# Kernel tuning notes

Measured on AMD Instinct MI355X. Metric: run time of the kernel, lower is better.

Reference implementation:

```python
import jax, jax.numpy as jnp
import numpy as np

D_MODEL = 768
N_HEADS = 8
HEAD_DIM = D_MODEL // N_HEADS
LN_EPS = 1e-5

def setup_inputs() -> dict:
    key = jax.random.key(0)
    k1, k2, k3 = jax.random.split(key, 3)
    B, L = 8, 4096
    x = jax.random.normal(k1, (B, L, D_MODEL), dtype=jnp.float32)
    gamma = jnp.ones((D_MODEL,), dtype=jnp.float32)
    beta = jnp.zeros((D_MODEL,), dtype=jnp.float32)
    # torch Linear weights transposed so forward is x @ W
    w_qkv = jax.random.normal(k2, (D_MODEL, 3 * D_MODEL), dtype=jnp.float32) * (1.0 / np.sqrt(D_MODEL))
    w_out = jax.random.normal(k3, (D_MODEL, D_MODEL), dtype=jnp.float32) * (1.0 / np.sqrt(D_MODEL))
    return {"x": x, "gamma": gamma, "beta": beta, "w_qkv": w_qkv, "w_out": w_out}

def reference(x, gamma, beta, w_qkv, w_out):
    B, L, D = x.shape
    residual = x
    # LayerNorm
    mu = jnp.mean(x, axis=-1, keepdims=True)
    var = jnp.mean(jnp.square(x - mu), axis=-1, keepdims=True)
    xn = (x - mu) * jax.lax.rsqrt(var + LN_EPS) * gamma + beta
    # qkv projection, split, reshape to [B, H, L, d]
    qkv = xn @ w_qkv  # [B, L, 3D]
    q, k, v = jnp.split(qkv, 3, axis=-1)
    def to_heads(t):
        return t.reshape(B, L, N_HEADS, HEAD_DIM).transpose(0, 2, 1, 3)
    q, k, v = to_heads(q), to_heads(k), to_heads(v)
    # feature maps: elu + 1
    q = jax.nn.elu(q) + 1.0
    k = jax.nn.elu(k) + 1.0
    # linear attention: kv aggregation then query readout
    kv = jnp.einsum('bhld,bhlv->bhdv', k, v)          # [B,H,d,d]
    out = jnp.einsum('bhld,bhdv->bhlv', q, kv)         # [B,H,L,d]
    k_sum = jnp.sum(k, axis=2)                         # [B,H,d]
    normalizer = jnp.einsum('bhld,bhd->bhl', q, k_sum) # [B,H,L]
    normalizer = jnp.maximum(normalizer, 1e-6)
    out = out / normalizer[..., None]
    out = out.transpose(0, 2, 1, 3).reshape(B, L, D)
    out = out @ w_out
    return out + residual
```

## Files before the change

### kernel.cpp

```cpp
#include <hip/hip_runtime.h>
#include <stdint.h>

#define D_MODEL 768
#define N3      2304
#define NHEAD   8
#define DH      96
#define BATCH   8
#define SEQ     4096
#define ROWS    (BATCH*SEQ)
#define LN_EPS  1e-5f

typedef __attribute__((ext_vector_type(8))) __bf16 bf16x8;
typedef __attribute__((ext_vector_type(4))) float f32x4;
typedef __attribute__((ext_vector_type(8))) unsigned short ushort8;
typedef __attribute__((ext_vector_type(4))) unsigned short ushort4v;

__device__ __forceinline__ unsigned short f2bf(float f) {
  union { float f; unsigned int u; } v; v.f = f;
  unsigned int r = v.u + 0x7FFFu + ((v.u >> 16) & 1u);
  return (unsigned short)(r >> 16);
}
__device__ __forceinline__ float bf2f(unsigned short u) {
  union { unsigned int u; float f; } v; v.u = ((unsigned int)u) << 16;
  return v.f;
}

#define GLOBAL_LDS16(src, dst) \
  __builtin_amdgcn_global_load_lds((const __attribute__((address_space(1))) void*)(src), \
                                   (__attribute__((address_space(3))) void*)(dst), 16, 0, 0)

#define GATE(n) do { asm volatile("s_waitcnt vmcnt(" #n ")" ::: "memory"); \
                     __builtin_amdgcn_s_barrier(); asm volatile("" ::: "memory"); } while (0)

__global__ __launch_bounds__(256) void transpose_cast_kernel(
    const float* __restrict__ in, unsigned short* __restrict__ out, int R, int C) {
  __shared__ float tile[32][33];
  int c0 = blockIdx.x * 32, r0 = blockIdx.y * 32;
  int tx = threadIdx.x & 31, ty = threadIdx.x >> 5;
  #pragma unroll
  for (int i = ty; i < 32; i += 8)
    tile[i][tx] = in[(size_t)(r0 + i) * C + c0 + tx];
  __syncthreads();
  #pragma unroll
  for (int i = ty; i < 32; i += 8)
    out[(size_t)(c0 + i) * R + r0 + tx] = f2bf(tile[tx][i]);
}

__global__ __launch_bounds__(256) void ln_kernel(
    const float* __restrict__ x, const float* __restrict__ gamma,
    const float* __restrict__ beta, unsigned short* __restrict__ xn) {
  int wave = threadIdx.x >> 6, lane = threadIdx.x & 63;
  int row = blockIdx.x * 4 + wave;
  const float* xr = x + (size_t)row * D_MODEL;
  f32x4 v[3];
  float s = 0.f, sq = 0.f;
  #pragma unroll
  for (int i = 0; i < 3; ++i) {
    v[i] = *(const f32x4*)(xr + (i * 64 + lane) * 4);
    #pragma unroll
    for (int c = 0; c < 4; ++c) { s += v[i][c]; sq += v[i][c] * v[i][c]; }
  }
  #pragma unroll
  for (int o = 32; o; o >>= 1) {
    s  += __shfl_xor(s, o, 64);
    sq += __shfl_xor(sq, o, 64);
  }
  float mu  = s * (1.f / 768.f);
  float var = sq * (1.f / 768.f) - mu * mu;
  float rs  = rsqrtf(var + LN_EPS);
  #pragma unroll
  for (int i = 0; i < 3; ++i) {
    int col = (i * 64 + lane) * 4;
    ushort4v o;
    #pragma unroll
    for (int c = 0; c < 4; ++c)
      o[c] = f2bf((v[i][c] - mu) * rs * gamma[col + c] + beta[col + c]);
    *(ushort4v*)(xn + (size_t)row * D_MODEL + col) = o;
  }
}

__global__ __launch_bounds__(512, 2) void gemm_qkv_kernel(
    const unsigned short* __restrict__ A, const unsigned short* __restrict__ Bt,
    unsigned short* __restrict__ qb, unsigned short* __restrict__ kT,
    unsigned short* __restrict__ vT) {
  __shared__ unsigned short As[3 * 8192];
  __shared__ unsigned short Bs[3 * 8192];
  const int K = D_MODEL, NKT = 24, nbn = N3 / 256;
  int nwg = gridDim.x, id = blockIdx.x;
  int q8 = nwg >> 3;
  int wg = (id & 7) * q8 + (id >> 3);
  int bm = wg / nbn, bn = wg % nbn;

  const int lane = threadIdx.x & 63, wid = threadIdx.x >> 6;
  const int wm = wid >> 2, wn = wid & 3;
  const int l15 = lane & 15, hi = lane >> 4;
  const int colS = (hi ^ ((l15 >> 1) & 3)) << 3;
  const int srow = lane >> 2;
  const int scol = ((lane & 3) ^ ((lane >> 3) & 3)) << 3;

  auto stage = [&](unsigned short* dstBase, const unsigned short* G, int bOff,
                   int buf, int kt) {
    #pragma unroll
    for (int q = 0; q < 2; ++q) {
      const unsigned short* src =
          G + (size_t)(bOff * 256 + q * 128 + wid * 16 + srow) * K + kt * 32 + scol;
      GLOBAL_LDS16(src, dstBase + buf * 8192 + q * 4096 + wid * 512);
    }
  };

  f32x4 acc[8][4];
  #pragma unroll
  for (int i = 0; i < 8; ++i)
    #pragma unroll
    for (int j = 0; j < 4; ++j) acc[i][j] = (f32x4){0.f, 0.f, 0.f, 0.f};

#define QTILE(BUF, STG) do { \
    bf16x8 af[8], bv[4]; \
    _Pragma("unroll") for (int mf = 0; mf < 8; ++mf) \
      af[mf] = *(const bf16x8*)&As[(BUF) * 8192 + (wm * 128 + mf * 16 + l15) * 32 + colS]; \
    _Pragma("unroll") for (int nf = 0; nf < 4; ++nf) \
      bv[nf] = *(const bf16x8*)&Bs[(BUF) * 8192 + (wn * 64 + nf * 16 + l15) * 32 + colS]; \
    STG; \
    __builtin_amdgcn_s_setprio(1); \
    _Pragma("unroll") for (int mf = 0; mf < 8; ++mf) \
      _Pragma("unroll") for (int nf = 0; nf < 4; ++nf) \
        acc[mf][nf] = __builtin_amdgcn_mfma_f32_16x16x32_bf16( \
            af[mf], bv[nf], acc[mf][nf], 0, 0, 0); \
    __builtin_amdgcn_s_setprio(0); \
  } while (0)

  stage(As, A, bm, 0, 0); stage(Bs, Bt, bn, 0, 0);
  stage(As, A, bm, 1, 1); stage(Bs, Bt, bn, 1, 1);

  for (int it = 0; it < 7; ++it) {
    int T = 3 * it;
    GATE(4); QTILE(0, { stage(As, A, bm, 2, T + 2); stage(Bs, Bt, bn, 2, T + 2); });
    GATE(4); QTILE(1, { stage(As, A, bm, 0, T + 3); stage(Bs, Bt, bn, 0, T + 3); });
    GATE(4); QTILE(2, { stage(As, A, bm, 1, T + 4); stage(Bs, Bt, bn, 1, T + 4); });
  }
  GATE(4); QTILE(0, { stage(As, A, bm, 2, NKT - 1); stage(Bs, Bt, bn, 2, NKT - 1); });
  GATE(4); QTILE(1, {});
  GATE(0); QTILE(2, {});
#undef QTILE

  int r0 = bm * 256 + wm * 128, c0 = bn * 256 + wn * 64;
  #pragma unroll
  for (int mf = 0; mf < 8; ++mf) {
    int lr = r0 + mf * 16 + hi * 4;
    int b = lr >> 12, lloc = lr & 4095;
    #pragma unroll
    for (int nf = 0; nf < 4; ++nf) {
      int col = c0 + nf * 16 + l15;
      float vv[4];
      #pragma unroll
      for (int r = 0; r < 4; ++r) {
        float v = acc[mf][nf][r];
        if (col < 1536) v = (v > 0.f) ? v + 1.f : __expf(v);
        vv[r] = v;
      }
      if (col < 768) {
        #pragma unroll
        for (int r = 0; r < 4; ++r)
          qb[(size_t)(lr + r) * D_MODEL + col] = f2bf(vv[r]);
      } else {
        int cc = (col < 1536) ? col - 768 : col - 1536;
        int h = cc / 96, d = cc - h * 96;
        unsigned short* T = (col < 1536) ? kT : vT;
        ushort4v pk = {f2bf(vv[0]), f2bf(vv[1]), f2bf(vv[2]), f2bf(vv[3])};
        *(ushort4v*)&T[((size_t)(b * 8 + h) * 96 + d) * 4096 + lloc] = pk;
      }
    }
  }
}

__global__ __launch_bounds__(256, 3) void gemm_out_kernel(
    const unsigned short* __restrict__ A, const unsigned short* __restrict__ Bt,
    const float* __restrict__ resid, float* __restrict__ Cf) {
  __shared__ unsigned short As[3 * 4096];
  __shared__ unsigned short Bs[3 * 4096];
  const int K = D_MODEL, nbn = 6;
  int nwg = gridDim.x, id = blockIdx.x;
  int q8 = nwg >> 3;
  int wg = (id & 7) * q8 + (id >> 3);
  int bm = wg / nbn, bn = wg % nbn;

  const int lane = threadIdx.x & 63, wid = threadIdx.x >> 6;
  const int wm = wid >> 1, wn = wid & 1;
  const int l15 = lane & 15, hi = lane >> 4;
  const int colS = (hi ^ ((l15 >> 1) & 3)) << 3;
  const int srow = lane >> 2;
  const int scol = ((lane & 3) ^ ((lane >> 3) & 3)) << 3;

  const unsigned short* a0 = A  + (size_t)(bm * 128 +      wid * 16 + srow) * K + scol;
  const unsigned short* a1 = A  + (size_t)(bm * 128 + 64 + wid * 16 + srow) * K + scol;
  const unsigned short* b0 = Bt + (size_t)(bn * 128 +      wid * 16 + srow) * K + scol;
  const unsigned short* b1 = Bt + (size_t)(bn * 128 + 64 + wid * 16 + srow) * K + scol;
  auto stage = [&](int buf, int kt) {
    GLOBAL_LDS16(a0 + kt * 32, &As[buf * 4096 +        wid * 512]);
    GLOBAL_LDS16(a1 + kt * 32, &As[buf * 4096 + 2048 + wid * 512]);
    GLOBAL_LDS16(b0 + kt * 32, &Bs[buf * 4096 +        wid * 512]);
    GLOBAL_LDS16(b1 + kt * 32, &Bs[buf * 4096 + 2048 + wid * 512]);
  };

  f32x4 acc[4][4];
  #pragma unroll
  for (int i = 0; i < 4; ++i)
    #pragma unroll
    for (int j = 0; j < 4; ++j) acc[i][j] = (f32x4){0.f, 0.f, 0.f, 0.f};

#define HTILE(BUF, STG) do { \
    bf16x8 af[4], bv[4]; \
    _Pragma("unroll") for (int mf = 0; mf < 4; ++mf) \
      af[mf] = *(const bf16x8*)&As[(BUF) * 4096 + (wm * 64 + mf * 16 + l15) * 32 + colS]; \
    _Pragma("unroll") for (int nf = 0; nf < 4; ++nf) \
      bv[nf] = *(const bf16x8*)&Bs[(BUF) * 4096 + (wn * 64 + nf * 16 + l15) * 32 + colS]; \
    STG; \
    __builtin_amdgcn_s_setprio(1); \
    _Pragma("unroll") for (int mf = 0; mf < 4; ++mf) \
      _Pragma("unroll") for (int nf = 0; nf < 4; ++nf) \
        acc[mf][nf] = __builtin_amdgcn_mfma_f32_16x16x32_bf16( \
            af[mf], bv[nf], acc[mf][nf], 0, 0, 0); \
    __builtin_amdgcn_s_setprio(0); \
  } while (0)

  stage(0, 0); stage(1, 1);
  for (int it = 0; it < 7; ++it) {
    int T = 3 * it;
    GATE(4); HTILE(0, stage(2, T + 2));
    GATE(4); HTILE(1, stage(0, T + 3));
    GATE(4); HTILE(2, stage(1, T + 4));
  }
  GATE(4); HTILE(0, stage(2, 23));
  GATE(4); HTILE(1, {});
  GATE(0); HTILE(2, {});
#undef HTILE

  int r0 = bm * 128 + wm * 64, c0 = bn * 128 + wn * 64;
  #pragma unroll
  for (int mf = 0; mf < 4; ++mf)
    #pragma unroll
    for (int nf = 0; nf < 4; ++nf) {
      int col = c0 + nf * 16 + l15;
      #pragma unroll
      for (int r = 0; r < 4; ++r) {
        int row = r0 + mf * 16 + hi * 4 + r;
        Cf[(size_t)row * D_MODEL + col] =
            acc[mf][nf][r] + resid[(size_t)row * D_MODEL + col];
      }
    }
}

__global__ __launch_bounds__(256) void kvagg2_kernel(
    const unsigned short* __restrict__ kT, const unsigned short* __restrict__ vT,
    float* __restrict__ kvp) {
  __shared__ unsigned short KTs[3 * 6144];
  __shared__ unsigned short VTs[3 * 8192];
  int bh = blockIdx.x >> 2, chunk = blockIdx.x & 3;
  int tid = threadIdx.x;
  int lane = tid & 63, wid = tid >> 6;
  int l15 = lane & 15, hi = lane >> 4;

  #pragma unroll
  for (int i = 0; i < 3; ++i) {
    int s = i * 256 + tid;
    int buf = s >> 8, r = 96 + ((s >> 3) & 31), sl = s & 7;
    unsigned short val = (r == 96) ? (unsigned short)0x3F80 : (unsigned short)0;
    ushort8 v8 = {val, val, val, val, val, val, val, val};
    *(ushort8*)&VTs[buf * 8192 + r * 64 + sl * 8] = v8;
  }
  __syncthreads();

  const size_t kbase = ((size_t)bh * 96) * 4096 + chunk * 1024;
  auto stage = [&](int buf, int t) {
    #pragma unroll
    for (int i = 0; i < 3; ++i) {
      int sidx = i * 256 + tid;
      int row = sidx >> 3;
      int L = (sidx & 7) ^ (row & 7);
      size_t g = kbase + (size_t)row * 4096 + t * 64 + L * 8;
      GLOBAL_LDS16(kT + g, &KTs[buf * 6144 + (i * 256 + wid * 64) * 8]);
      GLOBAL_LDS16(vT + g, &VTs[buf * 8192 + (i * 256 + wid * 64) * 8]);
    }
  };

  f32x4 acc[6][2];
  #pragma unroll
  for (int i = 0; i < 6; ++i)
    #pragma unroll
    for (int j = 0; j < 2; ++j) acc[i][j] = (f32x4){0.f, 0.f, 0.f, 0.f};

#define KVTILE(BUF) do { \
    _Pragma("unroll") for (int kq = 0; kq < 2; ++kq) { \
      bf16x8 af[6], bv[2]; \
      _Pragma("unroll") for (int mf = 0; mf < 6; ++mf) { \
        int row = mf * 16 + l15; \
        af[mf] = *(const bf16x8*)&KTs[(BUF) * 6144 + row * 64 + ((kq * 4 + hi) ^ (row & 7)) * 8]; } \
      _Pragma("unroll") for (int nf = 0; nf < 2; ++nf) { \
        int row = wid * 32 + nf * 16 + l15; \
        bv[nf] = *(const bf16x8*)&VTs[(BUF) * 8192 + row * 64 + ((kq * 4 + hi) ^ (row & 7)) * 8]; } \
      __builtin_amdgcn_s_setprio(1); \
      _Pragma("unroll") for (int mf = 0; mf < 6; ++mf) \
        _Pragma("unroll") for (int nf = 0; nf < 2; ++nf) \
          acc[mf][nf] = __builtin_amdgcn_mfma_f32_16x16x32_bf16( \
              af[mf], bv[nf], acc[mf][nf], 0, 0, 0); \
      __builtin_amdgcn_s_setprio(0); \
    } } while (0)

  stage(0, 0); stage(1, 1);
  for (int t = 0; t < 14; ++t) {
    stage((t + 2) % 3, t + 2);
    GATE(12);
    KVTILE(t % 3);
  }
  GATE(6); KVTILE(2);
  GATE(0); KVTILE(0);
#undef KVTILE

  float* outp = kvp + ((size_t)bh * 4 + chunk) * (96 * 112);
  #pragma unroll
  for (int nf = 0; nf < 2; ++nf) {
    int e = wid * 32 + nf * 16 + l15;
    if (e < 112) {
      #pragma unroll
      for (int mf = 0; mf < 6; ++mf)
        #pragma unroll
        for (int r = 0; r < 4; ++r) {
          int d = mf * 16 + hi * 4 + r;
          outp[d * 112 + e] = acc[mf][nf][r];
        }
    }
  }
}

__global__ __launch_bounds__(256) void kvreduce_kernel(
    const float* __restrict__ kvp, unsigned short* __restrict__ kvTo) {
  int idx = blockIdx.x * 256 + threadIdx.x;
  if (idx >= 64 * 112 * 96) return;
  int d = idx % 96;
  int e = (idx / 96) % 112;
  int bh = idx / (96 * 112);
  float s = 0.f;
  #pragma unroll
  for (int c = 0; c < 4; ++c)
    s += kvp[(((size_t)bh * 4 + c) * 96 + d) * 112 + e];
  kvTo[idx] = f2bf(s);
}

__global__ __launch_bounds__(256) void readout_kernel(
    const unsigned short* __restrict__ qb, const unsigned short* __restrict__ kvT,
    unsigned short* __restrict__ attn) {
  __shared__ unsigned short Qs[128][104];
  __shared__ unsigned short Ks[112][104];
  int bh = blockIdx.x >> 5, lc = blockIdx.x & 31;
  int b = bh >> 3, h = bh & 7;
  int l0 = lc * 128;
  int wave = threadIdx.x >> 6, lane = threadIdx.x & 63;
  #pragma unroll
  for (int i = 0; i < 6; ++i) {
    int idx = i * 256 + threadIdx.x;
    int l = idx / 12, oc = idx % 12;
    size_t g = ((size_t)b * SEQ + l0 + l) * D_MODEL + h * DH + oc * 8;
    *(ushort8*)&Qs[l][oc * 8] = *(const ushort8*)(qb + g);
  }
  const unsigned short* kvbh = kvT + (size_t)bh * 112 * 96;
  #pragma unroll
  for (int i = 0; i < 6; ++i) {
    int idx = i * 256 + threadIdx.x;
    if (idx < 1344) {
      int e = idx / 12, oc = idx % 12;
      *(ushort8*)&Ks[e][oc * 8] = *(const ushort8*)(kvbh + e * 96 + oc * 8);
    }
  }
  __syncthreads();
  f32x4 acc[2][7];
  #pragma unroll
  for (int i = 0; i < 2; ++i)
    #pragma unroll
    for (int j = 0; j < 7; ++j) acc[i][j] = (f32x4){0.f, 0.f, 0.f, 0.f};
  #pragma unroll
  for (int kq = 0; kq < 3; ++kq) {
    int k0 = kq * 32 + (lane >> 4) * 8;
    bf16x8 af[2], bfv[7];
    #pragma unroll
    for (int i = 0; i < 2; ++i) af[i]  = *(const bf16x8*)&Qs[wave * 32 + i * 16 + (lane & 15)][k0];
    #pragma unroll
    for (int j = 0; j < 7; ++j) bfv[j] = *(const bf16x8*)&Ks[j * 16 + (lane & 15)][k0];
    #pragma unroll
    for (int i = 0; i < 2; ++i)
      #pragma unroll
      for (int j = 0; j < 7; ++j)
        acc[i][j] = __builtin_amdgcn_mfma_f32_16x16x32_bf16(af[i], bfv[j], acc[i][j], 0, 0, 0);
  }
  int g4 = lane >> 4;
  #pragma unroll
  for (int i = 0; i < 2; ++i) {
    #pragma unroll
    for (int r = 0; r < 4; ++r) {
      float nv = __shfl(acc[i][6][r], lane & 48, 64);
      float inv = 1.f / fmaxf(nv, 1e-6f);
      size_t orow = (size_t)b * SEQ + l0 + wave * 32 + i * 16 + g4 * 4 + r;
      #pragma unroll
      for (int j = 0; j < 6; ++j) {
        int col = h * DH + j * 16 + (lane & 15);
        attn[orow * D_MODEL + col] = f2bf(acc[i][j][r] * inv);
      }
    }
  }
}

extern "C" void kernel_launch(void* const* d_in, const int* in_sizes, int n_in,
                              void* d_out, int out_size, void* d_ws, size_t ws_size,
                              hipStream_t stream) {
  const float* x     = (const float*)d_in[0];
  const float* gamma = (const float*)d_in[1];
  const float* beta  = (const float*)d_in[2];
  const float* w_qkv = (const float*)d_in[3];
  const float* w_out = (const float*)d_in[4];
  float* out = (float*)d_out;

  char* ws = (char*)d_ws;
  size_t off = 0;
  auto alloc = [&](size_t bytes) -> void* {
    void* p = ws + off; off += (bytes + 255) & ~(size_t)255; return p;
  };
  unsigned short* xn    = (unsigned short*)alloc((size_t)ROWS * D_MODEL * 2);
  unsigned short* qb    = (unsigned short*)alloc((size_t)ROWS * D_MODEL * 2);
  unsigned short* kTb   = (unsigned short*)alloc((size_t)64 * 96 * SEQ * 2);
  unsigned short* vTb   = (unsigned short*)alloc((size_t)64 * 96 * SEQ * 2);
  unsigned short* wqkvT = (unsigned short*)alloc((size_t)N3 * D_MODEL * 2);
  unsigned short* woutT = (unsigned short*)alloc((size_t)D_MODEL * D_MODEL * 2);
  float* kvp            = (float*)alloc((size_t)256 * 96 * 112 * 4);
  unsigned short* kvT   = (unsigned short*)alloc((size_t)64 * 112 * 96 * 2);

  transpose_cast_kernel<<<dim3(N3 / 32, D_MODEL / 32), 256, 0, stream>>>(w_qkv, wqkvT, D_MODEL, N3);
  transpose_cast_kernel<<<dim3(D_MODEL / 32, D_MODEL / 32), 256, 0, stream>>>(w_out, woutT, D_MODEL, D_MODEL);
  ln_kernel<<<ROWS / 4, 256, 0, stream>>>(x, gamma, beta, xn);
  gemm_qkv_kernel<<<(ROWS / 256) * (N3 / 256), 512, 0, stream>>>(xn, wqkvT, qb, kTb, vTb);
  kvagg2_kernel<<<256, 256, 0, stream>>>(kTb, vTb, kvp);
  kvreduce_kernel<<<(64 * 112 * 96 + 255) / 256, 256, 0, stream>>>(kvp, kvT);
  readout_kernel<<<2048, 256, 0, stream>>>(qb, kvT, xn);
  gemm_out_kernel<<<(ROWS / 128) * (D_MODEL / 128), 256, 0, stream>>>(xn, woutT, x, out);
}
```

Measured before the change: 340.2 us.

## Restructure QKV GEMM into 8-phase ping-pong schedule with BK=64 double buffering

```diff
diff --git a/kernel.cpp b/kernel.cpp
--- a/kernel.cpp
+++ b/kernel.cpp
@@ -29,8 +29,11 @@
   __builtin_amdgcn_global_load_lds((const __attribute__((address_space(1))) void*)(src), \
                                    (__attribute__((address_space(3))) void*)(dst), 16, 0, 0)
 
+#define BAR2() do { asm volatile("" ::: "memory"); __builtin_amdgcn_s_barrier(); \
+                    asm volatile("" ::: "memory"); } while (0)
 #define GATE(n) do { asm volatile("s_waitcnt vmcnt(" #n ")" ::: "memory"); \
                      __builtin_amdgcn_s_barrier(); asm volatile("" ::: "memory"); } while (0)
+#define LGKM0() asm volatile("s_waitcnt lgkmcnt(0)" ::: "memory")
 
 __global__ __launch_bounds__(256) void transpose_cast_kernel(
     const float* __restrict__ in, unsigned short* __restrict__ out, int R, int C) {
@@ -79,13 +82,14 @@
   }
 }
 
-__global__ __launch_bounds__(512, 2) void gemm_qkv_kernel(
+__global__ __launch_bounds__(512, 2) void gemm_qkv8_kernel(
     const unsigned short* __restrict__ A, const unsigned short* __restrict__ Bt,
     unsigned short* __restrict__ qb, unsigned short* __restrict__ kT,
     unsigned short* __restrict__ vT) {
-  __shared__ unsigned short As[3 * 8192];
-  __shared__ unsigned short Bs[3 * 8192];
-  const int K = D_MODEL, NKT = 24, nbn = N3 / 256;
+  __shared__ unsigned short As[2 * 16384];
+  __shared__ unsigned short Bs[2 * 16384];
+  const int K = D_MODEL, NKT = 12, nbn = N3 / 256;
+
   int nwg = gridDim.x, id = blockIdx.x;
   int q8 = nwg >> 3;
   int wg = (id & 7) * q8 + (id >> 3);
@@ -94,83 +98,121 @@
   const int lane = threadIdx.x & 63, wid = threadIdx.x >> 6;
   const int wm = wid >> 2, wn = wid & 3;
   const int l15 = lane & 15, hi = lane >> 4;
-  const int colS = (hi ^ ((l15 >> 1) & 3)) << 3;
-  const int srow = lane >> 2;
-  const int scol = ((lane & 3) ^ ((lane >> 3) & 3)) << 3;
-
-  auto stage = [&](unsigned short* dstBase, const unsigned short* G, int bOff,
-                   int buf, int kt) {
+  const int rsw = (hi ^ (l15 & 7)) << 3;
+  const int scol = ((lane & 7) ^ (lane >> 3)) << 3;
+
+  auto stgA = [&](int buf, int h, int kt) {
     #pragma unroll
     for (int q = 0; q < 2; ++q) {
+      int rbase = h * 128 + q * 64 + wid * 8;
       const unsigned short* src =
-          G + (size_t)(bOff * 256 + q * 128 + wid * 16 + srow) * K + kt * 32 + scol;
-      GLOBAL_LDS16(src, dstBase + buf * 8192 + q * 4096 + wid * 512);
+          A + (size_t)(bm * 256 + rbase + (lane >> 3)) * K + kt * 64 + scol;
+      GLOBAL_LDS16(src, &As[buf * 16384 + rbase * 64]);
     }
   };
-
-  f32x4 acc[8][4];
-  #pragma unroll
-  for (int i = 0; i < 8; ++i)
-    #pragma unroll
-    for (int j = 0; j < 4; ++j) acc[i][j] = (f32x4){0.f, 0.f, 0.f, 0.f};
-
-#define QTILE(BUF, STG) do { \
-    bf16x8 af[8], bv[4]; \
-    _Pragma("unroll") for (int mf = 0; mf < 8; ++mf) \
-      af[mf] = *(const bf16x8*)&As[(BUF) * 8192 + (wm * 128 + mf * 16 + l15) * 32 + colS]; \
-    _Pragma("unroll") for (int nf = 0; nf < 4; ++nf) \
-      bv[nf] = *(const bf16x8*)&Bs[(BUF) * 8192 + (wn * 64 + nf * 16 + l15) * 32 + colS]; \
-    STG; \
-    __builtin_amdgcn_s_setprio(1); \
-    _Pragma("unroll") for (int mf = 0; mf < 8; ++mf) \
-      _Pragma("unroll") for (int nf = 0; nf < 4; ++nf) \
-        acc[mf][nf] = __builtin_amdgcn_mfma_f32_16x16x32_bf16( \
-            af[mf], bv[nf], acc[mf][nf], 0, 0, 0); \
-    __builtin_amdgcn_s_setprio(0); \
-  } while (0)
-
-  stage(As, A, bm, 0, 0); stage(Bs, Bt, bn, 0, 0);
-  stage(As, A, bm, 1, 1); stage(Bs, Bt, bn, 1, 1);
-
-  for (int it = 0; it < 7; ++it) {
-    int T = 3 * it;
-    GATE(4); QTILE(0, { stage(As, A, bm, 2, T + 2); stage(Bs, Bt, bn, 2, T + 2); });
-    GATE(4); QTILE(1, { stage(As, A, bm, 0, T + 3); stage(Bs, Bt, bn, 0, T + 3); });
-    GATE(4); QTILE(2, { stage(As, A, bm, 1, T + 4); stage(Bs, Bt, bn, 1, T + 4); });
-  }
-  GATE(4); QTILE(0, { stage(As, A, bm, 2, NKT - 1); stage(Bs, Bt, bn, 2, NKT - 1); });
-  GATE(4); QTILE(1, {});
-  GATE(0); QTILE(2, {});
-#undef QTILE
-
-  int r0 = bm * 256 + wm * 128, c0 = bn * 256 + wn * 64;
-  #pragma unroll
-  for (int mf = 0; mf < 8; ++mf) {
-    int lr = r0 + mf * 16 + hi * 4;
-    int b = lr >> 12, lloc = lr & 4095;
-    #pragma unroll
-    for (int nf = 0; nf < 4; ++nf) {
-      int col = c0 + nf * 16 + l15;
-      float vv[4];
-      #pragma unroll
-      for (int r = 0; r < 4; ++r) {
-        float v = acc[mf][nf][r];
-        if (col < 1536) v = (v > 0.f) ? v + 1.f : __expf(v);
-        vv[r] = v;
-      }
-      if (col < 768) {
+  auto stgB = [&](int buf, int h, int kt) {
+    #pragma unroll
+    for (int q = 0; q < 2; ++q) {
+      int rbase = h * 128 + q * 64 + wid * 8;
+      const unsigned short* src =
+          Bt + (size_t)(bn * 256 + rbase + (lane >> 3)) * K + kt * 64 + scol;
+      GLOBAL_LDS16(src, &Bs[buf * 16384 + rbase * 64]);
+    }
+  };
+
+  f32x4 acc[2][4][2][2];
+  #pragma unroll
+  for (int a = 0; a < 2; ++a)
+    #pragma unroll
+    for (int b = 0; b < 4; ++b)
+      #pragma unroll
+      for (int c = 0; c < 2; ++c)
         #pragma unroll
-        for (int r = 0; r < 4; ++r)
-          qb[(size_t)(lr + r) * D_MODEL + col] = f2bf(vv[r]);
-      } else {
-        int cc = (col < 1536) ? col - 768 : col - 1536;
-        int h = cc / 96, d = cc - h * 96;
-        unsigned short* T = (col < 1536) ? kT : vT;
-        ushort4v pk = {f2bf(vv[0]), f2bf(vv[1]), f2bf(vv[2]), f2bf(vv[3])};
-        *(ushort4v*)&T[((size_t)(b * 8 + h) * 96 + d) * 4096 + lloc] = pk;
-      }
-    }
-  }
+        for (int d = 0; d < 2; ++d) acc[a][b][c][d] = (f32x4){0.f, 0.f, 0.f, 0.f};
+
+  bf16x8 af[4][2], bv0[2][2], bv1[2][2];
+
+#define RDA(BUF, QM) do { _Pragma("unroll") \
+  for (int mf = 0; mf < 4; ++mf) { \
+    int r = wm * 128 + (QM) * 64 + mf * 16 + l15; \
+    int base = (BUF) * 16384 + r * 64 + rsw; \
+    af[mf][0] = *(const bf16x8*)&As[base]; \
+    af[mf][1] = *(const bf16x8*)&As[base ^ 32]; } } while (0)
+#define RDB(BUF, QN, BV) do { _Pragma("unroll") \
+  for (int nf = 0; nf < 2; ++nf) { \
+    int r = wn * 64 + (QN) * 32 + nf * 16 + l15; \
+    int base = (BUF) * 16384 + r * 64 + rsw; \
+    BV[nf][0] = *(const bf16x8*)&Bs[base]; \
+    BV[nf][1] = *(const bf16x8*)&Bs[base ^ 32]; } } while (0)
+#define MM(QM, QN, BV) do { __builtin_amdgcn_s_setprio(1); \
+  _Pragma("unroll") for (int mf = 0; mf < 4; ++mf) \
+  _Pragma("unroll") for (int nf = 0; nf < 2; ++nf) { \
+    acc[QM][mf][QN][nf] = __builtin_amdgcn_mfma_f32_16x16x32_bf16( \
+        af[mf][0], BV[nf][0], acc[QM][mf][QN][nf], 0, 0, 0); \
+    acc[QM][mf][QN][nf] = __builtin_amdgcn_mfma_f32_16x16x32_bf16( \
+        af[mf][1], BV[nf][1], acc[QM][mf][QN][nf], 0, 0, 0); } \
+  __builtin_amdgcn_s_setprio(0); } while (0)
+
+  stgA(0, 0, 0); stgA(0, 1, 0); stgB(0, 0, 0); stgB(0, 1, 0);
+  stgB(1, 0, 1); stgB(1, 1, 1);
+  GATE(4);
+
+  const int NITER = NKT >> 1;
+  for (int it = 0; it < NITER - 1; ++it) {
+    int T = 2 * it;
+    RDA(0, 0); RDB(0, 0, bv0); stgA(1, 0, T + 1); BAR2(); LGKM0(); MM(0, 0, bv0); BAR2();
+    RDB(0, 1, bv1);            stgA(1, 1, T + 1); BAR2(); LGKM0(); MM(0, 1, bv1); BAR2();
+    RDA(0, 1);                 stgB(0, 0, T + 2); BAR2(); LGKM0(); MM(1, 1, bv1); BAR2();
+                               stgB(0, 1, T + 2); BAR2();          MM(1, 0, bv0); GATE(4);
+    RDA(1, 0); RDB(1, 0, bv0); stgA(0, 0, T + 2); BAR2(); LGKM0(); MM(0, 0, bv0); BAR2();
+    RDB(1, 1, bv1);            stgA(0, 1, T + 2); BAR2(); LGKM0(); MM(0, 1, bv1); BAR2();
+    RDA(1, 1);                 stgB(1, 0, T + 3); BAR2(); LGKM0(); MM(1, 1, bv1); BAR2();
+                               stgB(1, 1, T + 3); BAR2();          MM(1, 0, bv0); GATE(4);
+  }
+  RDA(0, 0); RDB(0, 0, bv0); stgA(1, 0, NKT - 1); BAR2(); LGKM0(); MM(0, 0, bv0); BAR2();
+  RDB(0, 1, bv1);            stgA(1, 1, NKT - 1); BAR2(); LGKM0(); MM(0, 1, bv1); BAR2();
+  RDA(0, 1);                                      BAR2(); LGKM0(); MM(1, 1, bv1); BAR2();
+                                                  BAR2();          MM(1, 0, bv0); GATE(0);
+  RDA(1, 0); RDB(1, 0, bv0);                      BAR2(); LGKM0(); MM(0, 0, bv0); BAR2();
+  RDB(1, 1, bv1);                                 BAR2(); LGKM0(); MM(0, 1, bv1); BAR2();
+  RDA(1, 1);                                      BAR2(); LGKM0(); MM(1, 1, bv1); BAR2();
+                                                  BAR2();          MM(1, 0, bv0);
+#undef RDA
+#undef RDB
+#undef MM
+
+  int r0 = bm * 256 + wm * 128, c0b = bn * 256 + wn * 64;
+  #pragma unroll
+  for (int qm = 0; qm < 2; ++qm)
+    #pragma unroll
+    for (int mf = 0; mf < 4; ++mf) {
+      int lr = r0 + qm * 64 + mf * 16 + hi * 4;
+      int b = lr >> 12, lloc = lr & 4095;
+      #pragma unroll
+      for (int qn = 0; qn < 2; ++qn)
+        #pragma unroll
+        for (int nf = 0; nf < 2; ++nf) {
+          int col = c0b + qn * 32 + nf * 16 + l15;
+          float vv[4];
+          #pragma unroll
+          for (int r = 0; r < 4; ++r) {
+            float v = acc[qm][mf][qn][nf][r];
+            if (col < 1536) v = (v > 0.f) ? v + 1.f : __expf(v);
+            vv[r] = v;
+          }
+          if (col < 768) {
+            #pragma unroll
+            for (int r = 0; r < 4; ++r)
+              qb[(size_t)(lr + r) * D_MODEL + col] = f2bf(vv[r]);
+          } else {
+            int cc = (col < 1536) ? col - 768 : col - 1536;
+            int h = cc / 96, d = cc - h * 96;
+            unsigned short* T = (col < 1536) ? kT : vT;
+            ushort4v pk = {f2bf(vv[0]), f2bf(vv[1]), f2bf(vv[2]), f2bf(vv[3])};
+            *(ushort4v*)&T[((size_t)(b * 8 + h) * 96 + d) * 4096 + lloc] = pk;
+          }
+        }
+    }
 }
 
 __global__ __launch_bounds__(256, 3) void gemm_out_kernel(
@@ -435,7 +477,7 @@
   transpose_cast_kernel<<<dim3(N3 / 32, D_MODEL / 32), 256, 0, stream>>>(w_qkv, wqkvT, D_MODEL, N3);
   transpose_cast_kernel<<<dim3(D_MODEL / 32, D_MODEL / 32), 256, 0, stream>>>(w_out, woutT, D_MODEL, D_MODEL);
   ln_kernel<<<ROWS / 4, 256, 0, stream>>>(x, gamma, beta, xn);
-  gemm_qkv_kernel<<<(ROWS / 256) * (N3 / 256), 512, 0, stream>>>(xn, wqkvT, qb, kTb, vTb);
+  gemm_qkv8_kernel<<<(ROWS / 256) * (N3 / 256), 512, 0, stream>>>(xn, wqkvT, qb, kTb, vTb);
   kvagg2_kernel<<<256, 256, 0, stream>>>(kTb, vTb, kvp);
   kvreduce_kernel<<<(64 * 112 * 96 + 255) / 256, 256, 0, stream>>>(kvp, kvT);
   readout_kernel<<<2048, 256, 0, stream>>>(qb, kvT, xn);
```

After: 342.6 us. Within noise of the previous version (+0.7%).

## Shrink QKV GEMM tile to 128x128 with 4 waves and specialized epilogues

Applied to the files above, without the earlier changes.

```diff
diff --git a/kernel.cpp b/kernel.cpp
--- a/kernel.cpp
+++ b/kernel.cpp
@@ -79,94 +79,103 @@
   }
 }
 
-__global__ __launch_bounds__(512, 2) void gemm_qkv_kernel(
+__global__ __launch_bounds__(256, 3) void gemm_qkv128_kernel(
     const unsigned short* __restrict__ A, const unsigned short* __restrict__ Bt,
     unsigned short* __restrict__ qb, unsigned short* __restrict__ kT,
     unsigned short* __restrict__ vT) {
-  __shared__ unsigned short As[3 * 8192];
-  __shared__ unsigned short Bs[3 * 8192];
-  const int K = D_MODEL, NKT = 24, nbn = N3 / 256;
+  __shared__ unsigned short As[3 * 4096];
+  __shared__ unsigned short Bs[3 * 4096];
+  const int K = D_MODEL, nbn = 18;
   int nwg = gridDim.x, id = blockIdx.x;
   int q8 = nwg >> 3;
   int wg = (id & 7) * q8 + (id >> 3);
   int bm = wg / nbn, bn = wg % nbn;
 
   const int lane = threadIdx.x & 63, wid = threadIdx.x >> 6;
-  const int wm = wid >> 2, wn = wid & 3;
+  const int wm = wid >> 1, wn = wid & 1;
   const int l15 = lane & 15, hi = lane >> 4;
   const int colS = (hi ^ ((l15 >> 1) & 3)) << 3;
   const int srow = lane >> 2;
   const int scol = ((lane & 3) ^ ((lane >> 3) & 3)) << 3;
 
-  auto stage = [&](unsigned short* dstBase, const unsigned short* G, int bOff,
-                   int buf, int kt) {
-    #pragma unroll
-    for (int q = 0; q < 2; ++q) {
-      const unsigned short* src =
-          G + (size_t)(bOff * 256 + q * 128 + wid * 16 + srow) * K + kt * 32 + scol;
-      GLOBAL_LDS16(src, dstBase + buf * 8192 + q * 4096 + wid * 512);
-    }
+  const unsigned short* a0 = A  + (size_t)(bm * 128 +      wid * 16 + srow) * K + scol;
+  const unsigned short* a1 = A  + (size_t)(bm * 128 + 64 + wid * 16 + srow) * K + scol;
+  const unsigned short* b0 = Bt + (size_t)(bn * 128 +      wid * 16 + srow) * K + scol;
+  const unsigned short* b1 = Bt + (size_t)(bn * 128 + 64 + wid * 16 + srow) * K + scol;
+  auto stage = [&](int buf, int kt) {
+    GLOBAL_LDS16(a0 + kt * 32, &As[buf * 4096 +        wid * 512]);
+    GLOBAL_LDS16(a1 + kt * 32, &As[buf * 4096 + 2048 + wid * 512]);
+    GLOBAL_LDS16(b0 + kt * 32, &Bs[buf * 4096 +        wid * 512]);
+    GLOBAL_LDS16(b1 + kt * 32, &Bs[buf * 4096 + 2048 + wid * 512]);
   };
 
-  f32x4 acc[8][4];
-  #pragma unroll
-  for (int i = 0; i < 8; ++i)
+  f32x4 acc[4][4];
+  #pragma unroll
+  for (int i = 0; i < 4; ++i)
     #pragma unroll
     for (int j = 0; j < 4; ++j) acc[i][j] = (f32x4){0.f, 0.f, 0.f, 0.f};
 
 #define QTILE(BUF, STG) do { \
-    bf16x8 af[8], bv[4]; \
-    _Pragma("unroll") for (int mf = 0; mf < 8; ++mf) \
-      af[mf] = *(const bf16x8*)&As[(BUF) * 8192 + (wm * 128 + mf * 16 + l15) * 32 + colS]; \
+    bf16x8 af[4], bv[4]; \
+    _Pragma("unroll") for (int mf = 0; mf < 4; ++mf) \
+      af[mf] = *(const bf16x8*)&As[(BUF) * 4096 + (wm * 64 + mf * 16 + l15) * 32 + colS]; \
     _Pragma("unroll") for (int nf = 0; nf < 4; ++nf) \
-      bv[nf] = *(const bf16x8*)&Bs[(BUF) * 8192 + (wn * 64 + nf * 16 + l15) * 32 + colS]; \
+      bv[nf] = *(const bf16x8*)&Bs[(BUF) * 4096 + (wn * 64 + nf * 16 + l15) * 32 + colS]; \
     STG; \
     __builtin_amdgcn_s_setprio(1); \
-    _Pragma("unroll") for (int mf = 0; mf < 8; ++mf) \
+    _Pragma("unroll") for (int mf = 0; mf < 4; ++mf) \
       _Pragma("unroll") for (int nf = 0; nf < 4; ++nf) \
         acc[mf][nf] = __builtin_amdgcn_mfma_f32_16x16x32_bf16( \
             af[mf], bv[nf], acc[mf][nf], 0, 0, 0); \
     __builtin_amdgcn_s_setprio(0); \
   } while (0)
 
-  stage(As, A, bm, 0, 0); stage(Bs, Bt, bn, 0, 0);
-  stage(As, A, bm, 1, 1); stage(Bs, Bt, bn, 1, 1);
-
+  stage(0, 0); stage(1, 1);
   for (int it = 0; it < 7; ++it) {
     int T = 3 * it;
-    GATE(4); QTILE(0, { stage(As, A, bm, 2, T + 2); stage(Bs, Bt, bn, 2, T + 2); });
-    GATE(4); QTILE(1, { stage(As, A, bm, 0, T + 3); stage(Bs, Bt, bn, 0, T + 3); });
-    GATE(4); QTILE(2, { stage(As, A, bm, 1, T + 4); stage(Bs, Bt, bn, 1, T + 4); });
-  }
-  GATE(4); QTILE(0, { stage(As, A, bm, 2, NKT - 1); stage(Bs, Bt, bn, 2, NKT - 1); });
+    GATE(4); QTILE(0, stage(2, T + 2));
+    GATE(4); QTILE(1, stage(0, T + 3));
+    GATE(4); QTILE(2, stage(1, T + 4));
+  }
+  GATE(4); QTILE(0, stage(2, 23));
   GATE(4); QTILE(1, {});
   GATE(0); QTILE(2, {});
 #undef QTILE
 
-  int r0 = bm * 256 + wm * 128, c0 = bn * 256 + wn * 64;
-  #pragma unroll
-  for (int mf = 0; mf < 8; ++mf) {
-    int lr = r0 + mf * 16 + hi * 4;
-    int b = lr >> 12, lloc = lr & 4095;
-    #pragma unroll
-    for (int nf = 0; nf < 4; ++nf) {
-      int col = c0 + nf * 16 + l15;
-      float vv[4];
-      #pragma unroll
-      for (int r = 0; r < 4; ++r) {
-        float v = acc[mf][nf][r];
-        if (col < 1536) v = (v > 0.f) ? v + 1.f : __expf(v);
-        vv[r] = v;
+  int r0 = bm * 128 + wm * 64, c0 = bn * 128 + wn * 64;
+  if (bn < 6) {
+    #pragma unroll
+    for (int mf = 0; mf < 4; ++mf)
+      #pragma unroll
+      for (int nf = 0; nf < 4; ++nf) {
+        int col = c0 + nf * 16 + l15;
+        #pragma unroll
+        for (int r = 0; r < 4; ++r) {
+          int row = r0 + mf * 16 + hi * 4 + r;
+          float v = acc[mf][nf][r];
+          v = (v > 0.f) ? v + 1.f : __expf(v);
+          qb[(size_t)row * D_MODEL + col] = f2bf(v);
+        }
       }
-      if (col < 768) {
+  } else {
+    const bool isK = (bn < 12);
+    unsigned short* T = isK ? kT : vT;
+    int cbase = c0 - (isK ? 768 : 1536);
+    #pragma unroll
+    for (int mf = 0; mf < 4; ++mf) {
+      int lr = r0 + mf * 16 + hi * 4;
+      int b = lr >> 12, lloc = lr & 4095;
+      #pragma unroll
+      for (int nf = 0; nf < 4; ++nf) {
+        int cc = cbase + nf * 16 + l15;
+        int h = cc / 96, d = cc - h * 96;
+        ushort4v pk;
         #pragma unroll
-        for (int r = 0; r < 4; ++r)
-          qb[(size_t)(lr + r) * D_MODEL + col] = f2bf(vv[r]);
-      } else {
-        int cc = (col < 1536) ? col - 768 : col - 1536;
-        int h = cc / 96, d = cc - h * 96;
-        unsigned short* T = (col < 1536) ? kT : vT;
-        ushort4v pk = {f2bf(vv[0]), f2bf(vv[1]), f2bf(vv[2]), f2bf(vv[3])};
+        for (int r = 0; r < 4; ++r) {
+          float v = acc[mf][nf][r];
+          if (isK) v = (v > 0.f) ? v + 1.f : __expf(v);
+          pk[r] = f2bf(v);
+        }
         *(ushort4v*)&T[((size_t)(b * 8 + h) * 96 + d) * 4096 + lloc] = pk;
       }
     }
@@ -435,7 +444,7 @@
   transpose_cast_kernel<<<dim3(N3 / 32, D_MODEL / 32), 256, 0, stream>>>(w_qkv, wqkvT, D_MODEL, N3);
   transpose_cast_kernel<<<dim3(D_MODEL / 32, D_MODEL / 32), 256, 0, stream>>>(w_out, woutT, D_MODEL, D_MODEL);
   ln_kernel<<<ROWS / 4, 256, 0, stream>>>(x, gamma, beta, xn);
-  gemm_qkv_kernel<<<(ROWS / 256) * (N3 / 256), 512, 0, stream>>>(xn, wqkvT, qb, kTb, vTb);
+  gemm_qkv128_kernel<<<(ROWS / 128) * (N3 / 128), 256, 0, stream>>>(xn, wqkvT, qb, kTb, vTb);
   kvagg2_kernel<<<256, 256, 0, stream>>>(kTb, vTb, kvp);
   kvreduce_kernel<<<(64 * 112 * 96 + 255) / 256, 256, 0, stream>>>(kvp, kvT);
   readout_kernel<<<2048, 256, 0, stream>>>(qb, kvT, xn);
```

After: 336.3 us. About the same (-1.2%).
